# Performance work log

Measured on AMD Instinct MI355X. Metric: run time of the kernel, lower is better.

The kernel has to match this reference:

```python
import jax, jax.numpy as jnp
import numpy as np

K_STEPS = 2  # number of staged propagation levels encoded in edge_mask


def _propagate(h, src, dst, mask, num_nodes):
    """KPropagate: K staged scatter-add steps over the edge list.

    Step k sums messages along edges with edge_mask == k; later steps
    propagate the freshly aggregated values (rule-node fan-out).
    """
    out = jnp.zeros_like(h)
    cur = h
    for k in range(K_STEPS):
        msg = jnp.where((mask == k)[:, None], cur[src], jnp.zeros((), h.dtype))  # [E, F]
        out = out + jax.ops.segment_sum(msg, dst, num_segments=num_nodes)
        cur = out
    return out


def setup_inputs() -> dict:
    key = jax.random.key(0)
    ks = jax.random.split(key, 8)
    V, R = 50000, 10000
    N = V + R
    E = 160000
    F_IN, F_OUT = 512, 128
    x = jax.random.normal(ks[0], (N, F_IN), dtype=jnp.float32)
    edge_index = jax.random.randint(ks[1], (2, E), 0, N, dtype=jnp.int64)
    edge_mask = jax.random.randint(ks[2], (E,), 0, K_STEPS, dtype=jnp.int64)
    # lin1: in_features -> in_features; lin2: in_features -> out_features
    s1 = 1.0 / np.sqrt(F_IN)
    W1 = jax.random.uniform(ks[3], (F_IN, F_IN), jnp.float32, -s1, s1)
    b1 = jax.random.uniform(ks[4], (F_IN,), jnp.float32, -s1, s1)
    W2 = jax.random.uniform(ks[5], (F_IN, F_OUT), jnp.float32, -s1, s1)
    b2 = jax.random.uniform(ks[6], (F_OUT,), jnp.float32, -s1, s1)
    return {"x": x, "edge_index": edge_index, "edge_mask": edge_mask,
            "vertex_cnt": V, "rule_cnt": R,
            "W1": W1, "b1": b1, "W2": W2, "b2": b2}


def reference(x, edge_index, edge_mask, vertex_cnt, rule_cnt, W1, b1, W2, b2):
    N = x.shape[0]  # == vertex_cnt + rule_cnt
    src, dst = edge_index[0], edge_index[1]
    h = x @ W1 + b1                                   # lin1
    h = jax.nn.relu(_propagate(h, src, dst, edge_mask, N))  # P1 -> relu
    h = h @ W2 + b2                                   # lin2
    h = _propagate(h, src, dst, edge_mask, N)         # P2
    # NOTE: original code computes log_softmax into `out` but returns x (=h).
    return h
```

## Files before the change

### kernel.cpp

```cpp
#include <hip/hip_runtime.h>

typedef __bf16 bf16x8 __attribute__((ext_vector_type(8)));
typedef float  floatx4 __attribute__((ext_vector_type(4)));
typedef unsigned short ushortx8 __attribute__((ext_vector_type(8)));
typedef unsigned short ushortx2 __attribute__((ext_vector_type(2)));

__device__ __forceinline__ float bf2f(unsigned short u) {
    return __uint_as_float(((unsigned)u) << 16);
}
__device__ __forceinline__ unsigned short f2bf(float f) {
    unsigned u = __float_as_uint(f);
    return (unsigned short)((u + 0x7FFFu + ((u >> 16) & 1u)) >> 16);
}

__device__ __forceinline__ void gload_lds16(const void* g, unsigned short* l) {
    __builtin_amdgcn_global_load_lds(
        (const __attribute__((address_space(1))) void*)g,
        (__attribute__((address_space(3))) void*)l, 16, 0, 0);
}

__global__ void transpose_cvt_kernel(const float* __restrict__ in,
                                     unsigned short* __restrict__ out,
                                     int K, int N) {
    int idx = blockIdx.x * blockDim.x + threadIdx.x;
    if (idx >= K * N) return;
    int k = idx / N, n = idx - k * N;
    out[n * K + k] = f2bf(in[idx]);
}

__global__ void zero_int_kernel(int* __restrict__ p, int n) {
    int i = blockIdx.x * blockDim.x + threadIdx.x;
    if (i < n) p[i] = 0;
}

#define ADJ_STRIDE 32
__global__ void build_csr_kernel(const int* __restrict__ ei, const int* __restrict__ em,
                                 int E, int Nn,
                                 int* __restrict__ cnt, int* __restrict__ adj) {
    int e = blockIdx.x * blockDim.x + threadIdx.x;
    if (e >= E) return;
    int d = ei[E + e];
    int m = em[e];
    int s = ei[e];
    int idx = m * Nn + d;
    int slot = atomicAdd(&cnt[idx], 1);
    if (slot < ADJ_STRIDE) adj[(size_t)idx * ADJ_STRIDE + slot] = s;
}

template<int NI, bool AF32>
__global__ __launch_bounds__(256) void gemm_glds(
    const void* __restrict__ Ap,
    const unsigned short* __restrict__ Bt,
    const float* __restrict__ bias,
    unsigned short* __restrict__ C,
    int M, int N, int K)
{
    constexpr int GB = 2 * NI;
    constexpr int AGROUPS = AF32 ? 32 : 16;
    constexpr int BGROUPS = 4 * NI;
    __shared__ unsigned short Sh[(AGROUPS + BGROUPS) * 512];
    unsigned short* Abase = Sh;
    unsigned short* Bbase = Sh + AGROUPS * 512;

    const int tid  = threadIdx.x;
    const int lane = tid & 63;
    const int wave = tid >> 6;

    int bx, by;
    {
        int gx = gridDim.x;
        int id = blockIdx.y * gx + blockIdx.x;
        int rows8 = gridDim.y & ~7;
        int full = rows8 * gx;
        if (id < full) {
            int per = gx * 8;
            int t = id / per, r = id - t * per;
            bx = r >> 3; by = t * 8 + (r & 7);
        } else {
            int t = id - full;
            by = rows8 + t / gx; bx = t - (t / gx) * gx;
        }
    }
    const int bM = by * 128;
    const int bN = bx * (NI * 32);
    const int wm = (wave >> 1) * 64;
    const int wn = (wave & 1) * (NI * 16);
    const int q    = lane >> 4;
    const int mrow = lane & 15;

    const float* pA32[8];
    const unsigned short* pA16[4];
    if (AF32) {
#pragma unroll
        for (int j = 0; j < 8; j++) {
            int gg = wave + 4 * j;
            int g = gg & 7, c = gg >> 3;
            int r = bM + g * 16 + mrow; if (r >= M) r = M - 1;
            pA32[j] = (const float*)Ap + (size_t)r * K + c * 16 + q * 4;
        }
    } else {
#pragma unroll
        for (int j = 0; j < 4; j++) {
            int gg = wave + 4 * j;
            int g = gg & 7, s = gg >> 3;
            int r = bM + g * 16 + mrow; if (r >= M) r = M - 1;
            pA16[j] = (const unsigned short*)Ap + (size_t)r * K + s * 32 + q * 8;
        }
    }
    const unsigned short* pB[NI];
#pragma unroll
    for (int c = 0; c < NI; c++) {
        int gg = wave + 4 * c;
        int g = gg & (GB - 1), s = gg / GB;
        pB[c] = Bt + (size_t)(bN + g * 16 + mrow) * K + s * 32 + q * 8;
    }

    floatx4 acc[4][NI];
#pragma unroll
    for (int i = 0; i < 4; i++)
#pragma unroll
        for (int j = 0; j < NI; j++) acc[i][j] = (floatx4)(0.0f);

    const int KI = K >> 6;
    for (int k = 0; k < KI; k++) {
        const int kt = k * 64;
        if (AF32) {
#pragma unroll
            for (int j = 0; j < 8; j++)
                gload_lds16(pA32[j] + kt, Abase + (wave + 4 * j) * 512);
        } else {
#pragma unroll
            for (int j = 0; j < 4; j++)
                gload_lds16(pA16[j] + kt, Abase + (wave + 4 * j) * 512);
        }
#pragma unroll
        for (int c = 0; c < NI; c++)
            gload_lds16(pB[c] + kt, Bbase + (wave + 4 * c) * 512);
        __syncthreads();

        bf16x8 af[2][4];
        if (AF32) {
#pragma unroll
            for (int s = 0; s < 2; s++)
#pragma unroll
                for (int mi = 0; mi < 4; mi++) {
                    const unsigned short* ap = Abase
                        + ((2 * s + (q >> 1)) * 8 + ((wave >> 1) * 4 + mi)) * 512
                        + (2 * (q & 1) * 16 + mrow) * 8;
                    floatx4 u0 = *(const floatx4*)ap;
                    floatx4 u1 = *(const floatx4*)(ap + 128);
                    bf16x8 t;
                    t[0] = (__bf16)u0[0]; t[1] = (__bf16)u0[1];
                    t[2] = (__bf16)u0[2]; t[3] = (__bf16)u0[3];
                    t[4] = (__bf16)u1[0]; t[5] = (__bf16)u1[1];
                    t[6] = (__bf16)u1[2]; t[7] = (__bf16)u1[3];
                    af[s][mi] = t;
                }
        } else {
#pragma unroll
            for (int s = 0; s < 2; s++)
#pragma unroll
                for (int mi = 0; mi < 4; mi++)
                    af[s][mi] = *(const bf16x8*)(Abase
                        + (s * 8 + (wave >> 1) * 4 + mi) * 512 + lane * 8);
        }

#pragma unroll
        for (int s = 0; s < 2; s++) {
            bf16x8 bfv[NI];
#pragma unroll
            for (int ni = 0; ni < NI; ni++)
                bfv[ni] = *(const bf16x8*)(Bbase
                    + (s * GB + (wave & 1) * NI + ni) * 512 + lane * 8);
#pragma unroll
            for (int mi = 0; mi < 4; mi++)
#pragma unroll
                for (int ni = 0; ni < NI; ni++)
                    acc[mi][ni] = __builtin_amdgcn_mfma_f32_16x16x32_bf16(
                        af[s][mi], bfv[ni], acc[mi][ni], 0, 0, 0);
        }
        __syncthreads();
    }

    constexpr int W = NI * 16;
    unsigned short* lbuf = Sh + wave * 32 * W;
    float bv[NI];
#pragma unroll
    for (int ni = 0; ni < NI; ni++) bv[ni] = bias[bN + wn + ni * 16 + mrow];

#pragma unroll
    for (int p = 0; p < 2; p++) {
#pragma unroll
        for (int mh = 0; mh < 2; mh++) {
            int mi = 2 * p + mh;
#pragma unroll
            for (int ni = 0; ni < NI; ni++)
#pragma unroll
                for (int r = 0; r < 4; r++)
                    lbuf[(mh * 16 + q * 4 + r) * W + ni * 16 + mrow] =
                        f2bf(acc[mi][ni][r] + bv[ni]);
        }
        constexpr int LPR = W / 8;
        constexpr int RPI = 64 / LPR;
#pragma unroll
        for (int i = 0; i < 32 / RPI; i++) {
            int prow = i * RPI + lane / LPR;
            int pcol = (lane % LPR) * 8;
            int grow = bM + wm + p * 32 + prow;
            if (grow < M)
                *(ushortx8*)(C + (size_t)grow * N + bN + wn + pcol) =
                    *(const ushortx8*)&lbuf[prow * W + pcol];
        }
    }
}

template <int VEC> struct VecT;
template <> struct VecT<8> { typedef ushortx8 type; };
template <> struct VecT<2> { typedef ushortx2 type; };

template <int VEC, bool ADD_SELF, bool RELU, bool OUT_F32>
__global__ __launch_bounds__(256) void prop_csr_kernel(
    const unsigned short* __restrict__ cur,
    void* __restrict__ outp,
    const int* __restrict__ cnt,
    const int* __restrict__ adj,
    int Nn)
{
    typedef typename VecT<VEC>::type VT;
    const int w = blockIdx.x * 4 + (threadIdx.x >> 6);
    if (w >= Nn) return;
    const int lane = threadIdx.x & 63;
    const int F = VEC * 64;
    const size_t off = (size_t)w * F + lane * VEC;

    int deg = cnt[w];
    if (deg > ADJ_STRIDE) deg = ADJ_STRIDE;
    const int* lst = adj + (size_t)w * ADJ_STRIDE;

    float acc[VEC];
    if (ADD_SELF) {
        VT v = *(const VT*)(cur + off);
#pragma unroll
        for (int i = 0; i < VEC; i++) acc[i] = bf2f(v[i]);
    } else {
#pragma unroll
        for (int i = 0; i < VEC; i++) acc[i] = 0.0f;
    }

    for (int i = 0; i < deg; i++) {
        int s = lst[i];
        VT v = *(const VT*)(cur + (size_t)s * F + lane * VEC);
#pragma unroll
        for (int j = 0; j < VEC; j++) acc[j] += bf2f(v[j]);
    }

#pragma unroll
    for (int i = 0; i < VEC; i++)
        if (RELU && acc[i] < 0.0f) acc[i] = 0.0f;

    if (OUT_F32) {
        float* out = (float*)outp;
        float2 o2;
#pragma unroll
        for (int i = 0; i < VEC; i += 2) {
            o2.x = acc[i]; o2.y = acc[i + 1];
            *(float2*)(out + off + i) = o2;
        }
    } else {
        VT o;
#pragma unroll
        for (int i = 0; i < VEC; i++) o[i] = f2bf(acc[i]);
        *(VT*)((unsigned short*)outp + off) = o;
    }
}

extern "C" void kernel_launch(void* const* d_in, const int* in_sizes, int n_in,
                              void* d_out, int out_size, void* d_ws, size_t ws_size,
                              hipStream_t stream)
{
    const float* x  = (const float*)d_in[0];
    const int*   ei = (const int*)d_in[1];
    const int*   em = (const int*)d_in[2];
    const float* W1 = (const float*)d_in[5];
    const float* b1 = (const float*)d_in[6];
    const float* W2 = (const float*)d_in[7];
    const float* b2 = (const float*)d_in[8];

    const int FIN = 512, FOUT = 128;
    const int Nn = in_sizes[0] / FIN;
    const int E  = in_sizes[2];

    char* ws = (char*)d_ws;
    size_t off = 0;
    auto alloc = [&](size_t bytes) -> char* {
        char* p = ws + off;
        off += (bytes + 255) & ~(size_t)255;
        return p;
    };
    unsigned short* W1t = (unsigned short*)alloc((size_t)FIN * FIN * 2);
    unsigned short* W2t = (unsigned short*)alloc((size_t)FIN * FOUT * 2);
    unsigned short* h1  = (unsigned short*)alloc((size_t)Nn * FIN * 2);
    unsigned short* A1  = (unsigned short*)alloc((size_t)Nn * FIN * 2);
    unsigned short* h2  = (unsigned short*)alloc((size_t)Nn * FOUT * 2);
    unsigned short* A2  = (unsigned short*)alloc((size_t)Nn * FOUT * 2);
    int* cnt = (int*)alloc((size_t)2 * Nn * 4);
    int* adj = (int*)alloc((size_t)2 * Nn * ADJ_STRIDE * 4);
    (void)ws_size; (void)n_in; (void)out_size;

    transpose_cvt_kernel<<<(FIN * FIN + 255) / 256, 256, 0, stream>>>(W1, W1t, FIN, FIN);
    transpose_cvt_kernel<<<(FIN * FOUT + 255) / 256, 256, 0, stream>>>(W2, W2t, FIN, FOUT);

    zero_int_kernel<<<(2 * Nn + 255) / 256, 256, 0, stream>>>(cnt, 2 * Nn);
    build_csr_kernel<<<(E + 255) / 256, 256, 0, stream>>>(ei, em, E, Nn, cnt, adj);

    const int gy = (Nn + 127) / 128;

    gemm_glds<4, true><<<dim3(FIN / 128, gy), 256, 0, stream>>>(
        (const void*)x, W1t, b1, h1, Nn, FIN, FIN);

    {
        int grid = (Nn + 3) / 4;
        prop_csr_kernel<8, false, false, false><<<grid, 256, 0, stream>>>(
            h1, A1, cnt, adj, Nn);
        prop_csr_kernel<8, true, true, false><<<grid, 256, 0, stream>>>(
            A1, h1, cnt + Nn, adj + (size_t)Nn * ADJ_STRIDE, Nn);
    }

    gemm_glds<2, false><<<dim3(FOUT / 64, gy), 256, 0, stream>>>(
        (const void*)h1, W2t, b2, h2, Nn, FOUT, FIN);

    {
        int grid = (Nn + 3) / 4;
        prop_csr_kernel<2, false, false, false><<<grid, 256, 0, stream>>>(
            h2, A2, cnt, adj, Nn);
        prop_csr_kernel<2, true, false, true><<<grid, 256, 0, stream>>>(
            A2, d_out, cnt + Nn, adj + (size_t)Nn * ADJ_STRIDE, Nn);
    }
}
```

Before: 419.3 us.

## Pre-convert x to bf16 and widen first GEMM tile to 256 columns

```diff
diff --git a/kernel.cpp b/kernel.cpp
--- a/kernel.cpp
+++ b/kernel.cpp
@@ -17,6 +17,18 @@
     __builtin_amdgcn_global_load_lds(
         (const __attribute__((address_space(1))) void*)g,
         (__attribute__((address_space(3))) void*)l, 16, 0, 0);
+}
+
+__global__ void cvt_f32_bf16_kernel(const float* __restrict__ in,
+                                    unsigned short* __restrict__ out, int n8) {
+    int i = blockIdx.x * blockDim.x + threadIdx.x;
+    if (i >= n8) return;
+    float4 v0 = ((const float4*)in)[2 * i];
+    float4 v1 = ((const float4*)in)[2 * i + 1];
+    ushortx8 o;
+    o[0] = f2bf(v0.x); o[1] = f2bf(v0.y); o[2] = f2bf(v0.z); o[3] = f2bf(v0.w);
+    o[4] = f2bf(v1.x); o[5] = f2bf(v1.y); o[6] = f2bf(v1.z); o[7] = f2bf(v1.w);
+    ((ushortx8*)out)[i] = o;
 }
 
 __global__ void transpose_cvt_kernel(const float* __restrict__ in,
@@ -47,20 +59,19 @@
     if (slot < ADJ_STRIDE) adj[(size_t)idx * ADJ_STRIDE + slot] = s;
 }
 
-template<int NI, bool AF32>
+template<int NI>
 __global__ __launch_bounds__(256) void gemm_glds(
-    const void* __restrict__ Ap,
+    const unsigned short* __restrict__ A,
     const unsigned short* __restrict__ Bt,
     const float* __restrict__ bias,
     unsigned short* __restrict__ C,
     int M, int N, int K)
 {
     constexpr int GB = 2 * NI;
-    constexpr int AGROUPS = AF32 ? 32 : 16;
     constexpr int BGROUPS = 4 * NI;
-    __shared__ unsigned short Sh[(AGROUPS + BGROUPS) * 512];
+    __shared__ unsigned short Sh[(16 + BGROUPS) * 512];
     unsigned short* Abase = Sh;
-    unsigned short* Bbase = Sh + AGROUPS * 512;
+    unsigned short* Bbase = Sh + 16 * 512;
 
     const int tid  = threadIdx.x;
     const int lane = tid & 63;
@@ -88,24 +99,13 @@
     const int q    = lane >> 4;
     const int mrow = lane & 15;
 
-    const float* pA32[8];
-    const unsigned short* pA16[4];
-    if (AF32) {
-#pragma unroll
-        for (int j = 0; j < 8; j++) {
-            int gg = wave + 4 * j;
-            int g = gg & 7, c = gg >> 3;
-            int r = bM + g * 16 + mrow; if (r >= M) r = M - 1;
-            pA32[j] = (const float*)Ap + (size_t)r * K + c * 16 + q * 4;
-        }
-    } else {
-#pragma unroll
-        for (int j = 0; j < 4; j++) {
-            int gg = wave + 4 * j;
-            int g = gg & 7, s = gg >> 3;
-            int r = bM + g * 16 + mrow; if (r >= M) r = M - 1;
-            pA16[j] = (const unsigned short*)Ap + (size_t)r * K + s * 32 + q * 8;
-        }
+    const unsigned short* pA[4];
+#pragma unroll
+    for (int j = 0; j < 4; j++) {
+        int gg = wave + 4 * j;
+        int g = gg & 7, s = gg >> 3;
+        int r = bM + g * 16 + mrow; if (r >= M) r = M - 1;
+        pA[j] = A + (size_t)r * K + s * 32 + q * 8;
     }
     const unsigned short* pB[NI];
 #pragma unroll
@@ -124,46 +124,21 @@
     const int KI = K >> 6;
     for (int k = 0; k < KI; k++) {
         const int kt = k * 64;
-        if (AF32) {
-#pragma unroll
-            for (int j = 0; j < 8; j++)
-                gload_lds16(pA32[j] + kt, Abase + (wave + 4 * j) * 512);
-        } else {
-#pragma unroll
-            for (int j = 0; j < 4; j++)
-                gload_lds16(pA16[j] + kt, Abase + (wave + 4 * j) * 512);
-        }
+#pragma unroll
+        for (int j = 0; j < 4; j++)
+            gload_lds16(pA[j] + kt, Abase + (wave + 4 * j) * 512);
 #pragma unroll
         for (int c = 0; c < NI; c++)
             gload_lds16(pB[c] + kt, Bbase + (wave + 4 * c) * 512);
         __syncthreads();
 
         bf16x8 af[2][4];
-        if (AF32) {
-#pragma unroll
-            for (int s = 0; s < 2; s++)
-#pragma unroll
-                for (int mi = 0; mi < 4; mi++) {
-                    const unsigned short* ap = Abase
-                        + ((2 * s + (q >> 1)) * 8 + ((wave >> 1) * 4 + mi)) * 512
-                        + (2 * (q & 1) * 16 + mrow) * 8;
-                    floatx4 u0 = *(const floatx4*)ap;
-                    floatx4 u1 = *(const floatx4*)(ap + 128);
-                    bf16x8 t;
-                    t[0] = (__bf16)u0[0]; t[1] = (__bf16)u0[1];
-                    t[2] = (__bf16)u0[2]; t[3] = (__bf16)u0[3];
-                    t[4] = (__bf16)u1[0]; t[5] = (__bf16)u1[1];
-                    t[6] = (__bf16)u1[2]; t[7] = (__bf16)u1[3];
-                    af[s][mi] = t;
-                }
-        } else {
-#pragma unroll
-            for (int s = 0; s < 2; s++)
-#pragma unroll
-                for (int mi = 0; mi < 4; mi++)
-                    af[s][mi] = *(const bf16x8*)(Abase
-                        + (s * 8 + (wave >> 1) * 4 + mi) * 512 + lane * 8);
-        }
+#pragma unroll
+        for (int s = 0; s < 2; s++)
+#pragma unroll
+            for (int mi = 0; mi < 4; mi++)
+                af[s][mi] = *(const bf16x8*)(Abase
+                    + (s * 8 + (wave >> 1) * 4 + mi) * 512 + lane * 8);
 
 #pragma unroll
         for (int s = 0; s < 2; s++) {
@@ -299,14 +274,16 @@
     };
     unsigned short* W1t = (unsigned short*)alloc((size_t)FIN * FIN * 2);
     unsigned short* W2t = (unsigned short*)alloc((size_t)FIN * FOUT * 2);
+    unsigned short* xb  = (unsigned short*)alloc((size_t)Nn * FIN * 2);
     unsigned short* h1  = (unsigned short*)alloc((size_t)Nn * FIN * 2);
-    unsigned short* A1  = (unsigned short*)alloc((size_t)Nn * FIN * 2);
     unsigned short* h2  = (unsigned short*)alloc((size_t)Nn * FOUT * 2);
     unsigned short* A2  = (unsigned short*)alloc((size_t)Nn * FOUT * 2);
     int* cnt = (int*)alloc((size_t)2 * Nn * 4);
     int* adj = (int*)alloc((size_t)2 * Nn * ADJ_STRIDE * 4);
+    unsigned short* A1 = xb;
     (void)ws_size; (void)n_in; (void)out_size;
 
+    cvt_f32_bf16_kernel<<<((Nn * FIN / 8) + 255) / 256, 256, 0, stream>>>(x, xb, Nn * FIN / 8);
     transpose_cvt_kernel<<<(FIN * FIN + 255) / 256, 256, 0, stream>>>(W1, W1t, FIN, FIN);
     transpose_cvt_kernel<<<(FIN * FOUT + 255) / 256, 256, 0, stream>>>(W2, W2t, FIN, FOUT);
 
@@ -315,8 +292,7 @@
 
     const int gy = (Nn + 127) / 128;
 
-    gemm_glds<4, true><<<dim3(FIN / 128, gy), 256, 0, stream>>>(
-        (const void*)x, W1t, b1, h1, Nn, FIN, FIN);
+    gemm_glds<8><<<dim3(FIN / 256, gy), 256, 0, stream>>>(xb, W1t, b1, h1, Nn, FIN, FIN);
 
     {
         int grid = (Nn + 3) / 4;
@@ -326,8 +302,7 @@
             A1, h1, cnt + Nn, adj + (size_t)Nn * ADJ_STRIDE, Nn);
     }
 
-    gemm_glds<2, false><<<dim3(FOUT / 64, gy), 256, 0, stream>>>(
-        (const void*)h1, W2t, b2, h2, Nn, FOUT, FIN);
+    gemm_glds<2><<<dim3(FOUT / 64, gy), 256, 0, stream>>>(h1, W2t, b2, h2, Nn, FOUT, FIN);
 
     {
         int grid = (Nn + 3) / 4;
```

Result: slower. 443.2 us (+5.7%).
